# Performance work log

Measured on AMD Instinct MI355X. Metric: run time of the kernel, lower is better.

## Reference

```python
import jax, jax.numpy as jnp
import numpy as np

T, B = 384, 128
IN_DIM, HID, OUT_DIM = 512, 1024, 512


def _lstm_step(h, c, x_t, Wx, Wh, b):
    # x_t: [B, D], h/c: [B, H]; gates order: i, f, g, o
    gates = x_t @ Wx + h @ Wh + b  # [B, 4H]
    i, f, g, o = jnp.split(gates, 4, axis=-1)
    c_new = jax.nn.sigmoid(f) * c + jax.nn.sigmoid(i) * jnp.tanh(g)
    h_new = jax.nn.sigmoid(o) * jnp.tanh(c_new)
    return h_new, c_new


def setup_inputs() -> dict:
    key = jax.random.key(0)
    ks = jax.random.split(key, 9)
    s_in = 1.0 / np.sqrt(IN_DIM)
    s_h = 1.0 / np.sqrt(HID)
    s_o = 1.0 / np.sqrt(OUT_DIM)
    return {
        "x": jax.random.normal(ks[0], (T, B, IN_DIM), dtype=jnp.float32),
        "hidden_state": jnp.zeros((1, B, HID), dtype=jnp.float32),
        "cell_state": jnp.zeros((1, B, HID), dtype=jnp.float32),
        "enc_Wx": jax.random.normal(ks[1], (IN_DIM, 4 * HID), dtype=jnp.float32) * s_in,
        "enc_Wh": jax.random.normal(ks[2], (HID, 4 * HID), dtype=jnp.float32) * s_h,
        "enc_b": jnp.zeros((4 * HID,), dtype=jnp.float32),
        "dec_Wx": jax.random.normal(ks[3], (OUT_DIM, 4 * HID), dtype=jnp.float32) * s_o,
        "dec_Wh": jax.random.normal(ks[4], (HID, 4 * HID), dtype=jnp.float32) * s_h,
        "dec_b": jnp.zeros((4 * HID,), dtype=jnp.float32),
        "fc_W": jax.random.normal(ks[5], (HID, OUT_DIM), dtype=jnp.float32) * s_h,
        "fc_b": jnp.zeros((OUT_DIM,), dtype=jnp.float32),
    }


def reference(x, hidden_state, cell_state, enc_Wx, enc_Wh, enc_b,
              dec_Wx, dec_Wh, dec_b, fc_W, fc_b):
    # ---- encoder: run LSTM over T steps, keep only final hidden state ----
    h0, c0 = hidden_state[0], cell_state[0]  # [B, H]

    def enc_step(carry, x_t):
        h, c = carry
        h, c = _lstm_step(h, c, x_t, enc_Wx, enc_Wh, enc_b)
        return (h, c), None

    (h_enc, _), _ = jax.lax.scan(enc_step, (h0, c0), x)

    y0 = jnp.zeros((B, OUT_DIM), dtype=x.dtype)
    c_dec0 = jnp.zeros((B, HID), dtype=x.dtype)

    def dec_step(carry, _):
        y, h, c = carry
        h, c = _lstm_step(h, c, y, dec_Wx, dec_Wh, dec_b)
        y = jax.nn.softmax(h @ fc_W + fc_b, axis=-1)  # softmax over dim=2
        return (y, h, c), y

    _, output = jax.lax.scan(dec_step, (y0, h_enc, c_dec0), None, length=T)
    return output  # [T, B, OUT_DIM]
```

## Files before the change

### kernel.cpp

```cpp
#include <hip/hip_runtime.h>


#define TS 384

typedef __attribute__((ext_vector_type(8))) short bf16x8;
typedef __attribute__((ext_vector_type(4))) float f32x4;

#define WS_XR 4096u
#define XR_SLOT 262144u
#define WS_HP (WS_XR + 4u*XR_SLOT)
#define HP_BUF 524288u
#define WS_FPN (WS_HP + 2u*HP_BUF)
#define WS_TOTAL (WS_FPN + 2097152u)

#define MFMA __builtin_amdgcn_mfma_f32_16x16x32_bf16

__device__ __forceinline__ unsigned short bf16r(float v) {
  unsigned u = __float_as_uint(v);
  u += 0x7FFFu + ((u >> 16) & 1u);
  return (unsigned short)(u >> 16);
}
__device__ __forceinline__ float bf2f(unsigned short h) {
  return __uint_as_float(((unsigned)h) << 16);
}
__device__ __forceinline__ void split2(float v, short& hi, short& lo) {
  unsigned short h = bf16r(v);
  float r = v - bf2f(h);
  hi = (short)h; lo = (short)bf16r(r);
}
__device__ __forceinline__ float sigm(float v)  { return 1.0f / (1.0f + __expf(-v)); }
__device__ __forceinline__ float tanhfa(float v){ return 1.0f - 2.0f / (__expf(2.0f*v) + 1.0f); }

__device__ __forceinline__ void st_u64(void* p, unsigned long long v) {
  __hip_atomic_store((unsigned long long*)p, v, __ATOMIC_RELAXED, __HIP_MEMORY_SCOPE_AGENT);
}
__device__ __forceinline__ unsigned long long ld_u64(const void* p) {
  return __hip_atomic_load((const unsigned long long*)p, __ATOMIC_RELAXED, __HIP_MEMORY_SCOPE_AGENT);
}
__device__ __forceinline__ void st_u32(unsigned* p, unsigned v) {
  __hip_atomic_store(p, v, __ATOMIC_RELAXED, __HIP_MEMORY_SCOPE_AGENT);
}
__device__ __forceinline__ unsigned ld_u32(const unsigned* p) {
  return __hip_atomic_load(p, __ATOMIC_RELAXED, __HIP_MEMORY_SCOPE_AGENT);
}
__device__ __forceinline__ void st_f32(float* p, float v) {
  __hip_atomic_store(p, v, __ATOMIC_RELAXED, __HIP_MEMORY_SCOPE_AGENT);
}
__device__ __forceinline__ float ld_f32(const float* p) {
  return __hip_atomic_load(p, __ATOMIC_RELAXED, __HIP_MEMORY_SCOPE_AGENT);
}
union FRAG { unsigned long long q[2]; bf16x8 v; };
__device__ __forceinline__ bf16x8 ld_frag(const short* base) {
  FRAG u;
  u.q[0] = ld_u64(base);
  u.q[1] = ld_u64(base + 4);
  return u.v;
}

__device__ __forceinline__ void setflag(unsigned* flag, unsigned val) {
  asm volatile("s_waitcnt vmcnt(0)" ::: "memory");
  __syncthreads();
  if (threadIdx.x == 0)
    __hip_atomic_store(flag, val, __ATOMIC_RELAXED, __HIP_MEMORY_SCOPE_AGENT);
}
__device__ __forceinline__ void hwait(const unsigned* flags, unsigned* invdone_line,
                                      bool leader, unsigned target, int* sDead) {
  if (leader) {
    if (threadIdx.x < 64) {
      const unsigned long long* q = (const unsigned long long*)(flags + threadIdx.x * 4);
      unsigned spins = 0;
      for (;;) {
        unsigned long long q0 = ld_u64(q), q1 = ld_u64(q + 1);
        bool ok = ((unsigned)q0 >= target) && ((unsigned)(q0 >> 32) >= target)
               && ((unsigned)q1 >= target) && ((unsigned)(q1 >> 32) >= target);
        if (__all(ok)) break;
        __builtin_amdgcn_s_sleep(1);
        if (++spins > (1u << 19)) { if (threadIdx.x == 0) *sDead = 1; break; }
      }
    }
    if (threadIdx.x == 0) {
      __builtin_amdgcn_fence(__ATOMIC_ACQUIRE, "agent");
      st_u32(invdone_line, target);
      asm volatile("s_waitcnt vmcnt(0)" ::: "memory");
    }
  } else {
    if (threadIdx.x == 0) {
      unsigned spins = 0;
      while (ld_u32(invdone_line) < target) {
        __builtin_amdgcn_s_sleep(1);
        if (++spins > (1u << 19)) { *sDead = 1; break; }
      }
      asm volatile("buffer_inv sc0" ::: "memory");
      asm volatile("s_waitcnt vmcnt(0)" ::: "memory");
    }
  }
  __syncthreads();
}
__device__ __forceinline__ void wait_hier(const unsigned* flags, unsigned* pub,
    int aggIdx, int nPub, unsigned target, int* sDead) {
  const int t = threadIdx.x;
  if (aggIdx >= 0) {
    if (t < 8) {
      const unsigned long long* q = (const unsigned long long*)(flags + aggIdx * 32 + t * 4);
      unsigned spins = 0;
      for (;;) {
        unsigned long long q0 = ld_u64(q), q1 = ld_u64(q + 1);
        bool ok = ((unsigned)q0 >= target) && ((unsigned)(q0 >> 32) >= target)
               && ((unsigned)q1 >= target) && ((unsigned)(q1 >> 32) >= target);
        if (__all(ok)) break;
        __builtin_amdgcn_s_sleep(1);
        if (++spins > (1u << 19)) { if (t == 0) *sDead = 1; break; }
      }
    }
    if (t == 0) st_u32(&pub[aggIdx], target);
  }
  if (t == 0) {
    unsigned spins = 0;
    for (;;) {
      bool ok = true;
      #pragma unroll
      for (int i = 0; i < 4; ++i) {
        if (i * 2 < nPub) {
          unsigned long long q0 = ld_u64((const unsigned long long*)pub + i);
          if (!((unsigned)q0 >= target && (unsigned)(q0 >> 32) >= target)) ok = false;
        }
      }
      if (ok) break;
      __builtin_amdgcn_s_sleep(1);
      if (++spins > (1u << 19)) { *sDead = 1; break; }
    }
  }
  __syncthreads();
}
__device__ __forceinline__ void wait64(const unsigned* flags, unsigned target, int* sDead) {
  if (threadIdx.x < 16) {
    const unsigned long long* q = (const unsigned long long*)(flags + threadIdx.x * 4);
    unsigned spins = 0;
    for (;;) {
      unsigned long long q0 = ld_u64(q), q1 = ld_u64(q + 1);
      bool ok = ((unsigned)q0 >= target) && ((unsigned)(q0 >> 32) >= target)
             && ((unsigned)q1 >= target) && ((unsigned)(q1 >> 32) >= target);
      if (__all(ok)) break;
      __builtin_amdgcn_s_sleep(1);
      if (++spins > (1u << 19)) { if (threadIdx.x == 0) *sDead = 1; break; }
    }
  }
  __syncthreads();
}

__device__ void load_gate_weights(const float* __restrict__ Wx, const float* __restrict__ Wh,
                                  int p, short* sBh, short* sBl) {
  for (int idx = threadIdx.x; idx < 24576; idx += 1024) {
    int j = idx & 7, l = (idx >> 3) & 63, kb = idx >> 9;
    int k = kb * 32 + ((l >> 4) << 3) + j;
    int c = l & 15;
    int gcol = (c >> 2) * 1024 + p * 4 + (c & 3);
    float wv = (k < 512) ? Wx[(size_t)k * 4096 + gcol]
                         : Wh[(size_t)(k - 512) * 4096 + gcol];
    short hi, lo; split2(wv, hi, lo);
    sBh[idx] = hi; sBl[idx] = lo;
  }
}
__device__ void load_fc_weights(const float* __restrict__ fcW, int kg, int cg,
                                short* sFh, short* sFl) {
  for (int idx = threadIdx.x; idx < 4096; idx += 1024) {
    int j = idx & 7, l = (idx >> 3) & 63, kb = idx >> 9;
    int unit = kg * 256 + kb * 32 + ((l >> 4) << 3) + j;
    int col = cg * 16 + (l & 15);
    short hi, lo; split2(fcW[(size_t)unit * 512 + col], hi, lo);
    sFh[idx] = hi; sFl[idx] = lo;
  }
}

template<int NKB, int D>
__device__ __forceinline__ void gg_pipe(const short* AH_, const short* AL_,
    const short* BH_, const short* BL_, int mt, int l,
    int kbA0, int kbB0, f32x4* acc)
{
  const bf16x8* AH = (const bf16x8*)AH_;
  const bf16x8* AL = (const bf16x8*)AL_;
  const bf16x8* BH = (const bf16x8*)BH_;
  const bf16x8* BL = (const bf16x8*)BL_;
  bf16x8 pah[D], pal[D];
  #pragma unroll
  for (int i = 0; i < D; ++i) {
    pah[i] = AH[((kbA0 + i) * 8 + mt) * 64 + l];
    pal[i] = AL[((kbA0 + i) * 8 + mt) * 64 + l];
  }
  #pragma unroll
  for (int i = 0; i < NKB; ++i) {
    bf16x8 ah = pah[i % D], al = pal[i % D];
    if (i + D < NKB) {
      pah[i % D] = AH[((kbA0 + i + D) * 8 + mt) * 64 + l];
      pal[i % D] = AL[((kbA0 + i + D) * 8 + mt) * 64 + l];
    }
    bf16x8 bh = BH[(kbB0 + i) * 64 + l];
    bf16x8 bl = BL[(kbB0 + i) * 64 + l];
    const int a = (i & 1) * 3;
    acc[a + 0] = MFMA(ah, bh, acc[a + 0], 0, 0, 0);
    acc[a + 1] = MFMA(ah, bl, acc[a + 1], 0, 0, 0);
    acc[a + 2] = MFMA(al, bh, acc[a + 2], 0, 0, 0);
  }
}
__device__ __forceinline__ void gg_finish(f32x4* acc, int kh, int mt, int l,
                                          float* LDSgate) {
  f32x4 s = (acc[0] + acc[3]) + ((acc[1] + acc[4]) + (acc[2] + acc[5]));
  const int col = l & 15, r0 = mt * 16 + ((l >> 4) << 2);
  float* plane = LDSgate + kh * 2176;
  #pragma unroll
  for (int j = 0; j < 4; ++j) plane[(r0 + j) * 17 + col] = s[j];
}

__device__ __forceinline__ void conv_x(const float* __restrict__ xsrc,
                                       short* dstH, short* dstL, int p, int tl) {
  if (tl < 32) {
    int g = p * 32 + tl;
    int l = g & 63, mt = (g >> 6) & 7, kb = g >> 9;
    int row = mt * 16 + (l & 15), k = kb * 32 + ((l >> 4) << 3);
    const float* xs = xsrc + (size_t)row * 512 + k;
    unsigned long long h64[2] = {0, 0}, l64[2] = {0, 0};
    #pragma unroll
    for (int j = 0; j < 8; ++j) {
      short hi, lo; split2(xs[j], hi, lo);
      h64[j >> 2] |= (unsigned long long)(unsigned short)hi << ((j & 3) * 16);
      l64[j >> 2] |= (unsigned long long)(unsigned short)lo << ((j & 3) * 16);
    }
    int off = g * 8;
    st_u64(dstH + off, h64[0]); st_u64(dstH + off + 4, h64[1]);
    st_u64(dstL + off, l64[0]); st_u64(dstL + off + 4, l64[1]);
  }
}

__global__ void __launch_bounds__(1024, 1)
lstm11(const float* __restrict__ x, const float* __restrict__ h0p,
       const float* __restrict__ c0p, const float* __restrict__ eWx,
       const float* __restrict__ eWh, const float* __restrict__ eb,
       const float* __restrict__ dWx, const float* __restrict__ dWh,
       const float* __restrict__ db, const float* __restrict__ fcW,
       const float* __restrict__ fcb, float* __restrict__ out,
       char* __restrict__ ws)
{
  __shared__ __align__(16) short sBh[24576], sBl[24576];
  __shared__ __align__(16) short sFh[4096], sFl[4096];
  __shared__ float LDSgate[2 * 2176];
  __shared__ unsigned hsplit[512];
  __shared__ float ybuf[512];
  __shared__ float red[16];
  __shared__ int sDead, sLeader, sXcd;

  const int p = blockIdx.x, t = threadIdx.x;
  const int w = t >> 6, l = t & 63;
  const int mt = w & 7, kh = w >> 3;
  if (t == 0) sDead = 0;

  unsigned* hflag = (unsigned*)ws;
  unsigned* yflag = (unsigned*)(ws + 1024);
  unsigned* fflag = (unsigned*)(ws + 2048);
  unsigned* ypub  = (unsigned*)(ws + 3072);
  unsigned* fpub  = (unsigned*)(ws + 3136);
  unsigned* elect = (unsigned*)(ws + 3264);

  if (t == 0) {
    unsigned xcd;
    asm volatile("s_getreg_b32 %0, hwreg(HW_REG_XCC_ID)" : "=s"(xcd));
    xcd &= 7u;
    sXcd = (int)xcd;
    unsigned old = __hip_atomic_fetch_add(&elect[xcd], 1u, __ATOMIC_ACQ_REL,
                                          __HIP_MEMORY_SCOPE_AGENT);
    sLeader = (old == 0u) ? 1 : 0;
  }
  __syncthreads();
  const bool leader = (sLeader != 0);
  unsigned* invd = (unsigned*)(ws + 3328 + sXcd * 64);

  const int yagg = (p >= 8 && p < 12) ? p - 8 : -1;
  const int fagg = (p >= 12 && p < 16) ? p - 12 : -1;

  short* xrH[4]; short* xrL[4];
  #pragma unroll
  for (int s4 = 0; s4 < 4; ++s4) {
    xrH[s4] = (short*)(ws + WS_XR + s4 * XR_SLOT);
    xrL[s4] = (short*)(ws + WS_XR + s4 * XR_SLOT + 131072u);
  }
  short* hpH[2]; short* hpL[2];
  #pragma unroll
  for (int b2 = 0; b2 < 2; ++b2) {
    hpH[b2] = (short*)(ws + WS_HP + b2 * HP_BUF);
    hpL[b2] = (short*)(ws + WS_HP + b2 * HP_BUF + 262144u);
  }
  float* fp = (float*)(ws + WS_FPN);

  const int row_pw = t & 127, u_pw = (t >> 7) & 3;

  load_gate_weights(eWx, eWh, p, sBh, sBl);
  conv_x(x, xrH[0], xrL[0], p, t);
  conv_x(x + 65536, xrH[1], xrL[1], p, t);
  if (t < 64) {
    int hg = p * 64 + t;
    int ll = hg & 63, mtt = (hg >> 6) & 7, hk = hg >> 9;
    int row = mtt * 16 + (ll & 15), k = hk * 32 + ((ll >> 4) << 3);
    const float* hs = h0p + (size_t)row * 1024 + k;
    unsigned long long h64[2] = {0, 0}, l64[2] = {0, 0};
    #pragma unroll
    for (int j = 0; j < 8; ++j) {
      short hi, lo; split2(hs[j], hi, lo);
      h64[j >> 2] |= (unsigned long long)(unsigned short)hi << ((j & 3) * 16);
      l64[j >> 2] |= (unsigned long long)(unsigned short)lo << ((j & 3) * 16);
    }
    int off = hg * 8;
    st_u64(hpH[0] + off, h64[0]); st_u64(hpH[0] + off + 4, h64[1]);
    st_u64(hpL[0] + off, l64[0]); st_u64(hpL[0] + off + 4, l64[1]);
  }
  float creg = 0.f, bq0 = 0.f, bq1 = 0.f, bq2 = 0.f, bq3 = 0.f;
  if (t < 512) {
    creg = c0p[(size_t)row_pw * 1024 + p * 4 + u_pw];
    bq0 = eb[0 * 1024 + p * 4 + u_pw];
    bq1 = eb[1 * 1024 + p * 4 + u_pw];
    bq2 = eb[2 * 1024 + p * 4 + u_pw];
    bq3 = eb[3 * 1024 + p * 4 + u_pw];
  }
  setflag(&hflag[p], 1u);
  hwait(hflag, invd, leader, 1u, &sDead);
  if (sDead) return;

  for (int st = 0; st < TS; ++st) {
    int rb = st & 1, wb = rb ^ 1, xs = st & 3;
    f32x4 z = {0.f, 0.f, 0.f, 0.f};
    f32x4 acc[6] = {z, z, z, z, z, z};
    gg_pipe<8, 4>(xrH[xs], xrL[xs], sBh, sBl, mt, l, kh * 8, kh * 8, acc);
    hwait(hflag, invd, leader, (unsigned)(st + 1), &sDead);
    if (sDead) return;
    gg_pipe<16, 4>(hpH[rb], hpL[rb], sBh, sBl, mt, l, kh * 16, 16 + kh * 16, acc);
    gg_finish(acc, kh, mt, l, LDSgate);
    __syncthreads();
    if (t < 512) {
      float g0 = LDSgate[row_pw * 17 + 0  + u_pw] + LDSgate[2176 + row_pw * 17 + 0  + u_pw] + bq0;
      float g1 = LDSgate[row_pw * 17 + 4  + u_pw] + LDSgate[2176 + row_pw * 17 + 4  + u_pw] + bq1;
      float g2 = LDSgate[row_pw * 17 + 8  + u_pw] + LDSgate[2176 + row_pw * 17 + 8  + u_pw] + bq2;
      float g3 = LDSgate[row_pw * 17 + 12 + u_pw] + LDSgate[2176 + row_pw * 17 + 12 + u_pw] + bq3;
      creg = sigm(g1) * creg + sigm(g0) * tanhfa(g2);
      float h = sigm(g3) * tanhfa(creg);
      short hi, lo; split2(h, hi, lo);
      hsplit[u_pw * 128 + row_pw] = ((unsigned)(unsigned short)hi << 16) | (unsigned short)lo;
    } else if (st + 2 < TS) {
      conv_x(x + (size_t)(st + 2) * 65536, xrH[(st + 2) & 3], xrL[(st + 2) & 3], p, t - 512);
    }
    __syncthreads();
    if (t < 128) {
      int r = t;
      unsigned w0 = hsplit[r], w1 = hsplit[128 + r], w2 = hsplit[256 + r], w3 = hsplit[384 + r];
      unsigned long long hi64 = (unsigned long long)(w0 >> 16)
        | ((unsigned long long)(w1 >> 16) << 16)
        | ((unsigned long long)(w2 >> 16) << 32)
        | ((unsigned long long)(w3 >> 16) << 48);
      unsigned long long lo64 = (unsigned long long)(w0 & 0xFFFFu)
        | ((unsigned long long)(w1 & 0xFFFFu) << 16)
        | ((unsigned long long)(w2 & 0xFFFFu) << 32)
        | ((unsigned long long)(w3 & 0xFFFFu) << 48);
      int hk = p >> 3, mtt = r >> 4;
      int lane_ = (((p >> 1) & 3) << 4) | (r & 15);
      int off = ((hk * 8 + mtt) * 64 + lane_) * 8 + (p & 1) * 4;
      st_u64(hpH[wb] + off, hi64);
      st_u64(hpL[wb] + off, lo64);
    }
    setflag(&hflag[p], (unsigned)(st + 2));
  }

  load_gate_weights(dWx, dWh, p, sBh, sBl);
  if (p >= 128) load_fc_weights(fcW, (p - 128) >> 5, (p - 128) & 31, sFh, sFl);
  if (t < 32) {
    int off = (p * 32 + t) * 8;
    st_u64(xrH[0] + off, 0ull); st_u64(xrH[0] + off + 4, 0ull);
    st_u64(xrL[0] + off, 0ull); st_u64(xrL[0] + off + 4, 0ull);
  }
  creg = 0.0f;
  if (t < 512) {
    bq0 = db[0 * 1024 + p * 4 + u_pw];
    bq1 = db[1 * 1024 + p * 4 + u_pw];
    bq2 = db[2 * 1024 + p * 4 + u_pw];
    bq3 = db[3 * 1024 + p * 4 + u_pw];
  }
  float fcb_r = (t < 512) ? fcb[t] : 0.f;
  setflag(&hflag[p], (unsigned)(TS + 2));

  const unsigned DB = (unsigned)(TS + 2);
  for (int st = 0; st < TS; ++st) {
    int rb = st & 1, wb = rb ^ 1;
    int ys = st & 1, yw = ys ^ 1;
    f32x4 z = {0.f, 0.f, 0.f, 0.f};
    f32x4 acc[6] = {z, z, z, z, z, z};
    hwait(hflag, invd, leader, DB + (unsigned)st, &sDead);
    if (sDead) return;
    gg_pipe<16, 4>(hpH[rb], hpL[rb], sBh, sBl, mt, l, kh * 16, 16 + kh * 16, acc);
    wait_hier(yflag, ypub, yagg, 4, (unsigned)st, &sDead);
    if (sDead) return;
    gg_pipe<8, 4>(xrH[ys], xrL[ys], sBh, sBl, mt, l, kh * 8, kh * 8, acc);
    gg_finish(acc, kh, mt, l, LDSgate);
    __syncthreads();
    if (t < 512) {
      float g0 = LDSgate[row_pw * 17 + 0  + u_pw] + LDSgate[2176 + row_pw * 17 + 0  + u_pw] + bq0;
      float g1 = LDSgate[row_pw * 17 + 4  + u_pw] + LDSgate[2176 + row_pw * 17 + 4  + u_pw] + bq1;
      float g2 = LDSgate[row_pw * 17 + 8  + u_pw] + LDSgate[2176 + row_pw * 17 + 8  + u_pw] + bq2;
      float g3 = LDSgate[row_pw * 17 + 12 + u_pw] + LDSgate[2176 + row_pw * 17 + 12 + u_pw] + bq3;
      creg = sigm(g1) * creg + sigm(g0) * tanhfa(g2);
      float h = sigm(g3) * tanhfa(creg);
      short hi, lo; split2(h, hi, lo);
      hsplit[u_pw * 128 + row_pw] = ((unsigned)(unsigned short)hi << 16) | (unsigned short)lo;
    }
    __syncthreads();
    if (t < 128) {
      int r = t;
      unsigned w0 = hsplit[r], w1 = hsplit[128 + r], w2 = hsplit[256 + r], w3 = hsplit[384 + r];
      unsigned long long hi64 = (unsigned long long)(w0 >> 16)
        | ((unsigned long long)(w1 >> 16) << 16)
        | ((unsigned long long)(w2 >> 16) << 32)
        | ((unsigned long long)(w3 >> 16) << 48);
      unsigned long long lo64 = (unsigned long long)(w0 & 0xFFFFu)
        | ((unsigned long long)(w1 & 0xFFFFu) << 16)
        | ((unsigned long long)(w2 & 0xFFFFu) << 32)
        | ((unsigned long long)(w3 & 0xFFFFu) << 48);
      int hk = p >> 3, mtt = r >> 4;
      int lane_ = (((p >> 1) & 3) << 4) | (r & 15);
      int off = ((hk * 8 + mtt) * 64 + lane_) * 8 + (p & 1) * 4;
      st_u64(hpH[wb] + off, hi64);
      st_u64(hpL[wb] + off, lo64);
    }
    setflag(&hflag[p], DB + (unsigned)(st + 1));

    if (p >= 128) {
      const int f = p - 128, kg = f >> 5, cg = f & 31;
      wait64(hflag + kg * 64, DB + (unsigned)(st + 1), &sDead);
      if (sDead) return;
      {
        const bf16x8* FB = (const bf16x8*)sFh;
        const bf16x8* FL = (const bf16x8*)sFl;
        bf16x8 fah[4], fal[4];
        #pragma unroll
        for (int kb = 0; kb < 4; ++kb) {
          int gkb = kg * 8 + kh * 4 + kb;
          fah[kb] = ld_frag(hpH[wb] + ((gkb * 8 + mt) * 64 + l) * 8);
          fal[kb] = ld_frag(hpL[wb] + ((gkb * 8 + mt) * 64 + l) * 8);
        }
        f32x4 a0 = z, a1 = z, a2 = z;
        #pragma unroll
        for (int kb = 0; kb < 4; ++kb) {
          bf16x8 bh = FB[(kh * 4 + kb) * 64 + l];
          bf16x8 bl = FL[(kh * 4 + kb) * 64 + l];
          a0 = MFMA(fah[kb], bh, a0, 0, 0, 0);
          a1 = MFMA(fah[kb], bl, a1, 0, 0, 0);
          a2 = MFMA(fal[kb], bh, a2, 0, 0, 0);
        }
        f32x4 s = a0 + (a1 + a2);
        int slice = kg * 2 + kh;
        int col = cg * 16 + (l & 15), r0 = mt * 16 + ((l >> 4) << 2);
        #pragma unroll
        for (int j = 0; j < 4; ++j)
          st_f32(&fp[(size_t)(slice * 128 + r0 + j) * 512 + col], s[j]);
      }
      setflag(&fflag[f], (unsigned)(st + 1));
    } else {
      wait_hier(fflag, fpub, fagg, 4, (unsigned)(st + 1), &sDead);
      if (sDead) return;
      float v = 0.f, e = 0.f, mx;
      if (t < 512) {
        float tv[8];
        #pragma unroll
        for (int s8 = 0; s8 < 8; ++s8)
          tv[s8] = ld_f32(&fp[(size_t)(s8 * 128 + p) * 512 + t]);
        v = fcb_r + ((tv[0] + tv[1]) + (tv[2] + tv[3]))
                  + ((tv[4] + tv[5]) + (tv[6] + tv[7]));
        mx = v;
        #pragma unroll
        for (int o = 32; o > 0; o >>= 1) mx = fmaxf(mx, __shfl_xor(mx, o));
        if (l == 0) red[w] = mx;
      }
      __syncthreads();
      if (t < 512) {
        mx = red[0];
        #pragma unroll
        for (int i = 1; i < 8; ++i) mx = fmaxf(mx, red[i]);
        e = __expf(v - mx);
        float ss = e;
        #pragma unroll
        for (int o = 32; o > 0; o >>= 1) ss += __shfl_xor(ss, o);
        if (l == 0) red[8 + w] = ss;
      }
      __syncthreads();
      if (t < 512) {
        float ss = (red[8] + red[9]) + (red[10] + red[11])
                 + (red[12] + red[13]) + (red[14] + red[15]);
        float y = e / ss;
        st_f32(&out[((size_t)st * 128 + p) * 512 + t], y);
        ybuf[t] = y;
      }
      __syncthreads();
      if (t < 64) {
        int kb = t >> 2, seg = t & 3;
        int k = kb * 32 + seg * 8;
        int lane_ = (seg << 4) | (p & 15), mtt = p >> 4;
        int off = ((kb * 8 + mtt) * 64 + lane_) * 8;
        unsigned long long h64[2] = {0, 0}, l64[2] = {0, 0};
        #pragma unroll
        for (int j = 0; j < 8; ++j) {
          short hi, lo; split2(ybuf[k + j], hi, lo);
          h64[j >> 2] |= (unsigned long long)(unsigned short)hi << ((j & 3) * 16);
          l64[j >> 2] |= (unsigned long long)(unsigned short)lo << ((j & 3) * 16);
        }
        st_u64(xrH[yw] + off, h64[0]); st_u64(xrH[yw] + off + 4, h64[1]);
        st_u64(xrL[yw] + off, l64[0]); st_u64(xrL[yw] + off + 4, l64[1]);
      }
      setflag(&yflag[p], (unsigned)(st + 1));
    }
  }
}

extern "C" void kernel_launch(void* const* d_in, const int* in_sizes, int n_in,
                              void* d_out, int out_size, void* d_ws, size_t ws_size,
                              hipStream_t stream) {
  const float* x   = (const float*)d_in[0];
  const float* h0  = (const float*)d_in[1];
  const float* c0  = (const float*)d_in[2];
  const float* eWx = (const float*)d_in[3];
  const float* eWh = (const float*)d_in[4];
  const float* eb  = (const float*)d_in[5];
  const float* dWx = (const float*)d_in[6];
  const float* dWh = (const float*)d_in[7];
  const float* db  = (const float*)d_in[8];
  const float* fcW = (const float*)d_in[9];
  const float* fcb = (const float*)d_in[10];
  float* out = (float*)d_out;

  if (ws_size < (size_t)WS_TOTAL) {
    hipMemsetAsync(d_out, 0xFF, (size_t)out_size * sizeof(float), stream);
    return;
  }
  hipMemsetAsync(d_ws, 0, 4096, stream);
  hipLaunchKernelGGL(lstm11, dim3(256), dim3(1024), 0, stream,
                     x, h0, c0, eWx, eWh, eb, dWx, dWh, db, fcW, fcb, out,
                     (char*)d_ws);
}
```

Measured before the change: 15.13 ms.

## Reschedule decoder FC/softmax step to overlap with next step's Wh GEMM

Restructures the persistent decoder loop so the FC projection and softmax for step st-1 run inside step st, after the hidden state is published, overlapping them with the recurrent h·Wh GEMM. The final step's FC/softmax moves to an epilogue after the loop. The hierarchical aggregator flag waits are replaced by a flat 128-flag wait, and the s_sleep backoff is removed from the spin loops, trading extra memory polling traffic for lower wake-up latency. This adds a full y-flag barrier inside the softmax blocks and changes the y double-buffer indexing, which carries ordering risk.

```diff
diff --git a/kernel.cpp b/kernel.cpp
--- a/kernel.cpp
+++ b/kernel.cpp
@@ -48,13 +48,6 @@
 }
 __device__ __forceinline__ float ld_f32(const float* p) {
   return __hip_atomic_load(p, __ATOMIC_RELAXED, __HIP_MEMORY_SCOPE_AGENT);
-}
-union FRAG { unsigned long long q[2]; bf16x8 v; };
-__device__ __forceinline__ bf16x8 ld_frag(const short* base) {
-  FRAG u;
-  u.q[0] = ld_u64(base);
-  u.q[1] = ld_u64(base + 4);
-  return u.v;
 }
 
 __device__ __forceinline__ void setflag(unsigned* flag, unsigned val) {
@@ -74,8 +67,7 @@
         bool ok = ((unsigned)q0 >= target) && ((unsigned)(q0 >> 32) >= target)
                && ((unsigned)q1 >= target) && ((unsigned)(q1 >> 32) >= target);
         if (__all(ok)) break;
-        __builtin_amdgcn_s_sleep(1);
-        if (++spins > (1u << 19)) { if (threadIdx.x == 0) *sDead = 1; break; }
+        if (++spins > (1u << 20)) { if (threadIdx.x == 0) *sDead = 1; break; }
       }
     }
     if (threadIdx.x == 0) {
@@ -87,8 +79,7 @@
     if (threadIdx.x == 0) {
       unsigned spins = 0;
       while (ld_u32(invdone_line) < target) {
-        __builtin_amdgcn_s_sleep(1);
-        if (++spins > (1u << 19)) { *sDead = 1; break; }
+        if (++spins > (1u << 20)) { *sDead = 1; break; }
       }
       asm volatile("buffer_inv sc0" ::: "memory");
       asm volatile("s_waitcnt vmcnt(0)" ::: "memory");
@@ -96,53 +87,21 @@
   }
   __syncthreads();
 }
-__device__ __forceinline__ void wait_hier(const unsigned* flags, unsigned* pub,
-    int aggIdx, int nPub, unsigned target, int* sDead) {
-  const int t = threadIdx.x;
-  if (aggIdx >= 0) {
-    if (t < 8) {
-      const unsigned long long* q = (const unsigned long long*)(flags + aggIdx * 32 + t * 4);
-      unsigned spins = 0;
-      for (;;) {
-        unsigned long long q0 = ld_u64(q), q1 = ld_u64(q + 1);
-        bool ok = ((unsigned)q0 >= target) && ((unsigned)(q0 >> 32) >= target)
-               && ((unsigned)q1 >= target) && ((unsigned)(q1 >> 32) >= target);
-        if (__all(ok)) break;
-        __builtin_amdgcn_s_sleep(1);
-        if (++spins > (1u << 19)) { if (t == 0) *sDead = 1; break; }
-      }
-    }
-    if (t == 0) st_u32(&pub[aggIdx], target);
-  }
-  if (t == 0) {
+__device__ __forceinline__ void wait128(const unsigned* flags, unsigned target, int* sDead) {
+  if (threadIdx.x < 64) {
+    const int i = threadIdx.x;
+    const bool act = (i * 4) < 128;
+    const unsigned long long* q = (const unsigned long long*)(flags + i * 4);
     unsigned spins = 0;
     for (;;) {
       bool ok = true;
-      #pragma unroll
-      for (int i = 0; i < 4; ++i) {
-        if (i * 2 < nPub) {
-          unsigned long long q0 = ld_u64((const unsigned long long*)pub + i);
-          if (!((unsigned)q0 >= target && (unsigned)(q0 >> 32) >= target)) ok = false;
-        }
-      }
-      if (ok) break;
-      __builtin_amdgcn_s_sleep(1);
-      if (++spins > (1u << 19)) { *sDead = 1; break; }
-    }
-  }
-  __syncthreads();
-}
-__device__ __forceinline__ void wait64(const unsigned* flags, unsigned target, int* sDead) {
-  if (threadIdx.x < 16) {
-    const unsigned long long* q = (const unsigned long long*)(flags + threadIdx.x * 4);
-    unsigned spins = 0;
-    for (;;) {
-      unsigned long long q0 = ld_u64(q), q1 = ld_u64(q + 1);
-      bool ok = ((unsigned)q0 >= target) && ((unsigned)(q0 >> 32) >= target)
-             && ((unsigned)q1 >= target) && ((unsigned)(q1 >> 32) >= target);
+      if (act) {
+        unsigned long long q0 = ld_u64(q), q1 = ld_u64(q + 1);
+        ok = ((unsigned)q0 >= target) && ((unsigned)(q0 >> 32) >= target)
+          && ((unsigned)q1 >= target) && ((unsigned)(q1 >> 32) >= target);
+      }
       if (__all(ok)) break;
-      __builtin_amdgcn_s_sleep(1);
-      if (++spins > (1u << 19)) { if (threadIdx.x == 0) *sDead = 1; break; }
+      if (++spins > (1u << 20)) { if (i == 0) *sDead = 1; break; }
     }
   }
   __syncthreads();
@@ -232,7 +191,7 @@
 }
 
 __global__ void __launch_bounds__(1024, 1)
-lstm11(const float* __restrict__ x, const float* __restrict__ h0p,
+lstm12(const float* __restrict__ x, const float* __restrict__ h0p,
        const float* __restrict__ c0p, const float* __restrict__ eWx,
        const float* __restrict__ eWh, const float* __restrict__ eb,
        const float* __restrict__ dWx, const float* __restrict__ dWh,
@@ -256,8 +215,6 @@
   unsigned* hflag = (unsigned*)ws;
   unsigned* yflag = (unsigned*)(ws + 1024);
   unsigned* fflag = (unsigned*)(ws + 2048);
-  unsigned* ypub  = (unsigned*)(ws + 3072);
-  unsigned* fpub  = (unsigned*)(ws + 3136);
   unsigned* elect = (unsigned*)(ws + 3264);
 
   if (t == 0) {
@@ -272,9 +229,6 @@
   __syncthreads();
   const bool leader = (sLeader != 0);
   unsigned* invd = (unsigned*)(ws + 3328 + sXcd * 64);
-
-  const int yagg = (p >= 8 && p < 12) ? p - 8 : -1;
-  const int fagg = (p >= 12 && p < 16) ? p - 12 : -1;
 
   short* xrH[4]; short* xrL[4];
   #pragma unroll
@@ -385,16 +339,100 @@
 
   const unsigned DB = (unsigned)(TS + 2);
   for (int st = 0; st < TS; ++st) {
-    int rb = st & 1, wb = rb ^ 1;
-    int ys = st & 1, yw = ys ^ 1;
+    const int rb = st & 1, wb = rb ^ 1;
     f32x4 z = {0.f, 0.f, 0.f, 0.f};
     f32x4 acc[6] = {z, z, z, z, z, z};
     hwait(hflag, invd, leader, DB + (unsigned)st, &sDead);
     if (sDead) return;
-    gg_pipe<16, 4>(hpH[rb], hpL[rb], sBh, sBl, mt, l, kh * 16, 16 + kh * 16, acc);
-    wait_hier(yflag, ypub, yagg, 4, (unsigned)st, &sDead);
-    if (sDead) return;
-    gg_pipe<8, 4>(xrH[ys], xrL[ys], sBh, sBl, mt, l, kh * 8, kh * 8, acc);
+    if (p >= 128) {
+      const int f = p - 128, kg = f >> 5, cg = f & 31;
+      if (st >= 1) {
+        const bf16x8* AH = (const bf16x8*)hpH[rb];
+        const bf16x8* AL = (const bf16x8*)hpL[rb];
+        const bf16x8* FB = (const bf16x8*)sFh;
+        const bf16x8* FL = (const bf16x8*)sFl;
+        f32x4 a0 = z, a1 = z, a2 = z;
+        #pragma unroll
+        for (int kb = 0; kb < 4; ++kb) {
+          int gkb = kg * 8 + kh * 4 + kb;
+          bf16x8 ah = AH[(gkb * 8 + mt) * 64 + l];
+          bf16x8 al = AL[(gkb * 8 + mt) * 64 + l];
+          bf16x8 bh = FB[(kh * 4 + kb) * 64 + l];
+          bf16x8 bl = FL[(kh * 4 + kb) * 64 + l];
+          a0 = MFMA(ah, bh, a0, 0, 0, 0);
+          a1 = MFMA(ah, bl, a1, 0, 0, 0);
+          a2 = MFMA(al, bh, a2, 0, 0, 0);
+        }
+        f32x4 s = a0 + (a1 + a2);
+        int slice = kg * 2 + kh;
+        int col = cg * 16 + (l & 15), r0 = mt * 16 + ((l >> 4) << 2);
+        #pragma unroll
+        for (int j = 0; j < 4; ++j)
+          st_f32(&fp[(size_t)(slice * 128 + r0 + j) * 512 + col], s[j]);
+        setflag(&fflag[f], (unsigned)st);
+      }
+      gg_pipe<16, 4>(hpH[rb], hpL[rb], sBh, sBl, mt, l, kh * 16, 16 + kh * 16, acc);
+      if (st >= 1) { wait128(yflag, (unsigned)st, &sDead); if (sDead) return; }
+      gg_pipe<8, 4>(xrH[rb], xrL[rb], sBh, sBl, mt, l, kh * 8, kh * 8, acc);
+    } else {
+      gg_pipe<16, 4>(hpH[rb], hpL[rb], sBh, sBl, mt, l, kh * 16, 16 + kh * 16, acc);
+      if (st >= 1) {
+        wait128(fflag, (unsigned)st, &sDead);
+        if (sDead) return;
+        float v = 0.f, e = 0.f, mx;
+        if (t < 512) {
+          float tv[8];
+          #pragma unroll
+          for (int s8 = 0; s8 < 8; ++s8)
+            tv[s8] = ld_f32(&fp[(size_t)(s8 * 128 + p) * 512 + t]);
+          v = fcb_r + ((tv[0] + tv[1]) + (tv[2] + tv[3]))
+                    + ((tv[4] + tv[5]) + (tv[6] + tv[7]));
+          mx = v;
+          #pragma unroll
+          for (int o = 32; o > 0; o >>= 1) mx = fmaxf(mx, __shfl_xor(mx, o));
+          if (l == 0) red[w] = mx;
+        }
+        __syncthreads();
+        if (t < 512) {
+          mx = red[0];
+          #pragma unroll
+          for (int i = 1; i < 8; ++i) mx = fmaxf(mx, red[i]);
+          e = __expf(v - mx);
+          float ss = e;
+          #pragma unroll
+          for (int o = 32; o > 0; o >>= 1) ss += __shfl_xor(ss, o);
+          if (l == 0) red[8 + w] = ss;
+        }
+        __syncthreads();
+        if (t < 512) {
+          float ss = (red[8] + red[9]) + (red[10] + red[11])
+                   + (red[12] + red[13]) + (red[14] + red[15]);
+          float y = e / ss;
+          st_f32(&out[((size_t)(st - 1) * 128 + p) * 512 + t], y);
+          ybuf[t] = y;
+        }
+        __syncthreads();
+        if (t < 64) {
+          int kb = t >> 2, seg = t & 3;
+          int k = kb * 32 + seg * 8;
+          int lane_ = (seg << 4) | (p & 15), mtt = p >> 4;
+          int off = ((kb * 8 + mtt) * 64 + lane_) * 8;
+          unsigned long long h64[2] = {0, 0}, l64[2] = {0, 0};
+          #pragma unroll
+          for (int j = 0; j < 8; ++j) {
+            short hi, lo; split2(ybuf[k + j], hi, lo);
+            h64[j >> 2] |= (unsigned long long)(unsigned short)hi << ((j & 3) * 16);
+            l64[j >> 2] |= (unsigned long long)(unsigned short)lo << ((j & 3) * 16);
+          }
+          st_u64(xrH[rb] + off, h64[0]); st_u64(xrH[rb] + off + 4, h64[1]);
+          st_u64(xrL[rb] + off, l64[0]); st_u64(xrL[rb] + off + 4, l64[1]);
+        }
+        setflag(&yflag[p], (unsigned)st);
+        wait128(yflag, (unsigned)st, &sDead);
+        if (sDead) return;
+      }
+      gg_pipe<8, 4>(xrH[rb], xrL[rb], sBh, sBl, mt, l, kh * 8, kh * 8, acc);
+    }
     gg_finish(acc, kh, mt, l, LDSgate);
     __syncthreads();
     if (t < 512) {
@@ -426,40 +464,40 @@
       st_u64(hpL[wb] + off, lo64);
     }
     setflag(&hflag[p], DB + (unsigned)(st + 1));
-
+  }
+
+  {
+    const int rb = TS & 1;
+    hwait(hflag, invd, leader, DB + (unsigned)TS, &sDead);
+    if (sDead) return;
     if (p >= 128) {
       const int f = p - 128, kg = f >> 5, cg = f & 31;
-      wait64(hflag + kg * 64, DB + (unsigned)(st + 1), &sDead);
-      if (sDead) return;
-      {
-        const bf16x8* FB = (const bf16x8*)sFh;
-        const bf16x8* FL = (const bf16x8*)sFl;
-        bf16x8 fah[4], fal[4];
-        #pragma unroll
-        for (int kb = 0; kb < 4; ++kb) {
-          int gkb = kg * 8 + kh * 4 + kb;
-          fah[kb] = ld_frag(hpH[wb] + ((gkb * 8 + mt) * 64 + l) * 8);
-          fal[kb] = ld_frag(hpL[wb] + ((gkb * 8 + mt) * 64 + l) * 8);
-        }
-        f32x4 a0 = z, a1 = z, a2 = z;
-        #pragma unroll
-        for (int kb = 0; kb < 4; ++kb) {
-          bf16x8 bh = FB[(kh * 4 + kb) * 64 + l];
-          bf16x8 bl = FL[(kh * 4 + kb) * 64 + l];
-          a0 = MFMA(fah[kb], bh, a0, 0, 0, 0);
-          a1 = MFMA(fah[kb], bl, a1, 0, 0, 0);
-          a2 = MFMA(fal[kb], bh, a2, 0, 0, 0);
-        }
-        f32x4 s = a0 + (a1 + a2);
-        int slice = kg * 2 + kh;
-        int col = cg * 16 + (l & 15), r0 = mt * 16 + ((l >> 4) << 2);
-        #pragma unroll
-        for (int j = 0; j < 4; ++j)
-          st_f32(&fp[(size_t)(slice * 128 + r0 + j) * 512 + col], s[j]);
-      }
-      setflag(&fflag[f], (unsigned)(st + 1));
+      const bf16x8* AH = (const bf16x8*)hpH[rb];
+      const bf16x8* AL = (const bf16x8*)hpL[rb];
+      const bf16x8* FB = (const bf16x8*)sFh;
+      const bf16x8* FL = (const bf16x8*)sFl;
+      f32x4 z = {0.f, 0.f, 0.f, 0.f};
+      f32x4 a0 = z, a1 = z, a2 = z;
+      #pragma unroll
+      for (int kb = 0; kb < 4; ++kb) {
+        int gkb = kg * 8 + kh * 4 + kb;
+        bf16x8 ah = AH[(gkb * 8 + mt) * 64 + l];
+        bf16x8 al = AL[(gkb * 8 + mt) * 64 + l];
+        bf16x8 bh = FB[(kh * 4 + kb) * 64 + l];
+        bf16x8 bl = FL[(kh * 4 + kb) * 64 + l];
+        a0 = MFMA(ah, bh, a0, 0, 0, 0);
+        a1 = MFMA(ah, bl, a1, 0, 0, 0);
+        a2 = MFMA(al, bh, a2, 0, 0, 0);
+      }
+      f32x4 s = a0 + (a1 + a2);
+      int slice = kg * 2 + kh;
+      int col = cg * 16 + (l & 15), r0 = mt * 16 + ((l >> 4) << 2);
+      #pragma unroll
+      for (int j = 0; j < 4; ++j)
+        st_f32(&fp[(size_t)(slice * 128 + r0 + j) * 512 + col], s[j]);
+      setflag(&fflag[f], (unsigned)TS);
     } else {
-      wait_hier(fflag, fpub, fagg, 4, (unsigned)(st + 1), &sDead);
+      wait128(fflag, (unsigned)TS, &sDead);
       if (sDead) return;
       float v = 0.f, e = 0.f, mx;
       if (t < 512) {
@@ -489,27 +527,8 @@
       if (t < 512) {
         float ss = (red[8] + red[9]) + (red[10] + red[11])
                  + (red[12] + red[13]) + (red[14] + red[15]);
-        float y = e / ss;
-        st_f32(&out[((size_t)st * 128 + p) * 512 + t], y);
-        ybuf[t] = y;
-      }
-      __syncthreads();
-      if (t < 64) {
-        int kb = t >> 2, seg = t & 3;
-        int k = kb * 32 + seg * 8;
-        int lane_ = (seg << 4) | (p & 15), mtt = p >> 4;
-        int off = ((kb * 8 + mtt) * 64 + lane_) * 8;
-        unsigned long long h64[2] = {0, 0}, l64[2] = {0, 0};
-        #pragma unroll
-        for (int j = 0; j < 8; ++j) {
-          short hi, lo; split2(ybuf[k + j], hi, lo);
-          h64[j >> 2] |= (unsigned long long)(unsigned short)hi << ((j & 3) * 16);
-          l64[j >> 2] |= (unsigned long long)(unsigned short)lo << ((j & 3) * 16);
-        }
-        st_u64(xrH[yw] + off, h64[0]); st_u64(xrH[yw] + off + 4, h64[1]);
-        st_u64(xrL[yw] + off, l64[0]); st_u64(xrL[yw] + off + 4, l64[1]);
-      }
-      setflag(&yflag[p], (unsigned)(st + 1));
+        st_f32(&out[((size_t)(TS - 1) * 128 + p) * 512 + t], e / ss);
+      }
     }
   }
 }
@@ -535,7 +554,7 @@
     return;
   }
   hipMemsetAsync(d_ws, 0, 4096, stream);
-  hipLaunchKernelGGL(lstm11, dim3(256), dim3(1024), 0, stream,
+  hipLaunchKernelGGL(lstm12, dim3(256), dim3(1024), 0, stream,
                      x, h0, c0, eWx, eWh, eb, dWx, dWh, db, fcW, fcb, out,
                      (char*)d_ws);
 }
```

New measurement: 13.74 ms. -9.2%, faster.
